# Kernel tuning notes

Hardware: AMD Instinct MI355X
Metric: run time of the kernel (lower is better)

## Reference

```python
import jax, jax.numpy as jnp
import numpy as np
from jax import lax

B, H, W, CIN = 16, 96, 320, 32
N_ACTIVE = 200000
COUT = 256
FC_IN = (H // 8) * (W // 8) * 128  # 12*40*128 = 61440


def _conv(x, w, b):
    # stride-2, pad-1, 3x3 conv in NCHW / OIHW layout
    y = lax.conv_general_dilated(x, w, (2, 2), [(1, 1), (1, 1)],
                                 dimension_numbers=('NCHW', 'OIHW', 'NCHW'))
    return y + b[None, :, None, None]


def _maxpool3(x):
    # 3x3 maxpool, stride 1, pad 1 (NCHW)
    return lax.reduce_window(x, -jnp.inf, lax.max,
                             (1, 1, 3, 3), (1, 1, 1, 1),
                             [(0, 0), (0, 0), (1, 1), (1, 1)])


def setup_inputs() -> dict:
    key = jax.random.key(0)
    ks = jax.random.split(key, 12)
    input_feat = jax.random.normal(ks[0], (B, H, W, CIN), dtype=jnp.float32)
    cb = jax.random.randint(ks[1], (N_ACTIVE, 1), 0, B)
    cy = jax.random.randint(ks[2], (N_ACTIVE, 1), 0, H)
    cx = jax.random.randint(ks[3], (N_ACTIVE, 1), 0, W)
    spconv_coords = jnp.concatenate([cb, cy, cx], axis=1).astype(jnp.int32)
    w1 = jax.random.normal(ks[4], (32, CIN, 3, 3), dtype=jnp.float32) * (1.0 / np.sqrt(CIN * 9))
    b1 = jax.random.normal(ks[5], (32,), dtype=jnp.float32) * 0.01
    w2 = jax.random.normal(ks[6], (64, 32, 3, 3), dtype=jnp.float32) * (1.0 / np.sqrt(32 * 9))
    b2 = jax.random.normal(ks[7], (64,), dtype=jnp.float32) * 0.01
    w3 = jax.random.normal(ks[8], (128, 64, 3, 3), dtype=jnp.float32) * (1.0 / np.sqrt(64 * 9))
    b3 = jax.random.normal(ks[9], (128,), dtype=jnp.float32) * 0.01
    fc_w = jax.random.normal(ks[10], (COUT, FC_IN), dtype=jnp.float32) * (1.0 / np.sqrt(FC_IN))
    fc_b = jax.random.normal(ks[11], (COUT,), dtype=jnp.float32) * 0.01
    return {"input_feat": input_feat, "spconv_coords": spconv_coords,
            "w1": w1, "b1": b1, "w2": w2, "b2": b2, "w3": w3, "b3": b3,
            "fc_w": fc_w, "fc_b": fc_b}


def reference(input_feat, spconv_coords, w1, b1, w2, b2, w3, b3, fc_w, fc_b):
    bi = spconv_coords[:, 0]
    yi = spconv_coords[:, 1]
    xi = spconv_coords[:, 2]
    # gather active-site features, then scatter into a dense NHWC grid
    feats = input_feat[bi, yi, xi]                       # [N, CIN]
    dense = jnp.zeros_like(input_feat).at[bi, yi, xi].set(feats)
    x = dense.transpose(0, 3, 1, 2)                      # [B, CIN, H, W]
    x = jax.nn.relu(_maxpool3(_conv(x, w1, b1)))         # [B, 32, H/2, W/2]
    x = jax.nn.relu(_maxpool3(_conv(x, w2, b2)))         # [B, 64, H/4, W/4]
    x = jax.nn.relu(_maxpool3(_conv(x, w3, b3)))         # [B, 128, H/8, W/8]
    x = x.reshape(x.shape[0], -1)                        # [B, FC_IN]
    return jax.nn.relu(x @ fc_w.T + fc_b)                # [B, COUT]
```

## Files before the change

### kernel.cpp

```cpp
#include <hip/hip_runtime.h>

#define NB 16
#define NH 96
#define NW 320
#define NCIN 32

#define FC_K 61440
#define FC_KC 120
#define FC_NCHUNK 512

typedef __attribute__((ext_vector_type(8))) short short8;
typedef __attribute__((ext_vector_type(4))) float f32x4;

__device__ inline unsigned short f2bf(float f) {
    union { float f; unsigned int u; } v; v.f = f;
    unsigned int r = v.u + 0x7FFF + ((v.u >> 16) & 1);
    return (unsigned short)(r >> 16);
}

__global__ __launch_bounds__(256) void setup_all(const float* __restrict__ w1,
                                                 const float* __restrict__ w2,
                                                 const float* __restrict__ w3,
                                                 unsigned short* __restrict__ f1,
                                                 unsigned short* __restrict__ f2,
                                                 unsigned short* __restrict__ f3,
                                                 const int* __restrict__ coords,
                                                 const float* __restrict__ input,
                                                 unsigned short* __restrict__ inBf,
                                                 int n) {
    if (blockIdx.x < 396) {
        int i = blockIdx.x * 256 + threadIdx.x;
        if (i < 9216) {
            int j = i & 7, lane = (i >> 3) & 63, nt = (i >> 9) & 1, tap = i >> 10;
            int ic = ((lane >> 4) * 8) + j, oc = nt * 16 + (lane & 15);
            f1[i] = f2bf(w1[(oc * 32 + ic) * 9 + tap]);
        } else if (i < 27648) {
            int v = i - 9216;
            int j = v & 7, lane = (v >> 3) & 63, nt = (v >> 9) & 3, tap = v >> 11;
            int ic = ((lane >> 4) * 8) + j, oc = nt * 16 + (lane & 15);
            f2[v] = f2bf(w2[(oc * 32 + ic) * 9 + tap]);
        } else if (i < 101376) {
            int v = i - 27648;
            int j = v & 7, lane = (v >> 3) & 63, nt = (v >> 9) & 7, kk = v >> 12;
            int tap = kk >> 1, ks = kk & 1;
            int ic = ks * 32 + ((lane >> 4) * 8) + j, oc = nt * 16 + (lane & 15);
            f3[v] = f2bf(w3[(oc * 64 + ic) * 9 + tap]);
        }
    } else {
        int i = (blockIdx.x - 396) * 256 + threadIdx.x;
        if (i >= n * 4) return;
        int ci = i >> 2, q = i & 3;
        int b = coords[ci * 3 + 0], y = coords[ci * 3 + 1], x = coords[ci * 3 + 2];
        long base = ((long)((b * NH + y) * NW + x)) * NCIN + q * 8;
        const float4* src = (const float4*)(input + base);
        float4 v0 = src[0], v1 = src[1];
        union { short8 s8; unsigned short us[8]; } o;
        o.us[0] = f2bf(v0.x); o.us[1] = f2bf(v0.y); o.us[2] = f2bf(v0.z); o.us[3] = f2bf(v0.w);
        o.us[4] = f2bf(v1.x); o.us[5] = f2bf(v1.y); o.us[6] = f2bf(v1.z); o.us[7] = f2bf(v1.w);
        *(short8*)(inBf + base) = o.s8;
    }
}

template<int IC, int OC, int NL, int IH, int IW, int OH, int OW>
__global__ __launch_bounds__(256) void conv_mfma(
    const unsigned short* __restrict__ inPtr,
    const unsigned short* __restrict__ wfrag,
    const float* __restrict__ bias,
    float* __restrict__ out)
{
    constexpr int KS = IC / 32;
    constexpr int NT = OC / 16;
    constexpr int NG = NT / NL;
    constexpr int NSTRIPS = NB * OH * OW / 16;

    const int wid  = (blockIdx.x * 256 + threadIdx.x) >> 6;
    const int lane = threadIdx.x & 63;
    const int ntb  = (wid % NG) * NL;
    const int s    = wid / NG;
    if (s >= NSTRIPS) return;
    const int quad = lane >> 4;
    const int lm   = lane & 15;

    const int p0 = s * 16;
    const int posA = p0 + lm;
    const int b  = posA / (OH * OW);
    const int rr = posA % (OH * OW);
    const int oy = rr / OW, ox = rr % OW;
    const int iy0 = oy * 2 - 1, ix0 = ox * 2 - 1;

    int cell[9];
    bool okb[9];
    #pragma unroll
    for (int t9 = 0; t9 < 9; t9++) {
        const int iy = iy0 + t9 / 3;
        const int ix = ix0 + t9 % 3;
        const bool ok = (iy >= 0) && (iy < IH) && (ix >= 0) && (ix < IW);
        cell[t9] = ok ? ((b * IH + iy) * IW + ix) : 0;
        okb[t9] = ok;
    }

    short8 zero8;
    #pragma unroll
    for (int j = 0; j < 8; j++) zero8[j] = 0;

    f32x4 acc[NL][2];
    #pragma unroll
    for (int nl = 0; nl < NL; nl++)
        #pragma unroll
        for (int pp = 0; pp < 2; pp++)
            acc[nl][pp] = (f32x4){0.f, 0.f, 0.f, 0.f};

    #pragma unroll 1
    for (int ks = 0; ks < KS; ks++) {
        short8 av[9];
        #pragma unroll
        for (int t9 = 0; t9 < 9; t9++) {
            short8 v = *(const short8*)(inPtr + (long)cell[t9] * IC + ks * 32 + quad * 8);
            av[t9] = okb[t9] ? v : zero8;
        }
        #pragma unroll
        for (int nl = 0; nl < NL; nl++) {
            #pragma unroll
            for (int t9 = 0; t9 < 9; t9++) {
                short8 bf = *(const short8*)(wfrag + (((t9 * KS + ks) * NT + ntb + nl) * 64 + lane) * 8);
                if (t9 & 1) acc[nl][1] = __builtin_amdgcn_mfma_f32_16x16x32_bf16(av[t9], bf, acc[nl][1], 0, 0, 0);
                else        acc[nl][0] = __builtin_amdgcn_mfma_f32_16x16x32_bf16(av[t9], bf, acc[nl][0], 0, 0, 0);
            }
        }
    }

    const long rowBase = (long)p0 + quad * 4;
    #pragma unroll
    for (int nl = 0; nl < NL; nl++) {
        const int oc = (ntb + nl) * 16 + lm;
        const float bv = bias[oc];
        #pragma unroll
        for (int reg = 0; reg < 4; reg++)
            out[(rowBase + reg) * OC + oc] = acc[nl][0][reg] + acc[nl][1][reg] + bv;
    }
}

template<int C, int HH, int WW, bool BF16OUT>
__global__ __launch_bounds__(256) void maxpool3_relu(const float* __restrict__ in, void* __restrict__ outv) {
    constexpr int C4 = C / 4;
    int i = blockIdx.x * blockDim.x + threadIdx.x;
    if (i >= NB * HH * WW * C4) return;
    int c = i % C4;
    int x = (i / C4) % WW;
    int y = (i / (C4 * WW)) % HH;
    int b = i / (C4 * WW * HH);
    float4 m = make_float4(-3.0e38f, -3.0e38f, -3.0e38f, -3.0e38f);
    #pragma unroll
    for (int dy = -1; dy <= 1; dy++) {
        int yy = y + dy;
        if (yy < 0 || yy >= HH) continue;
        #pragma unroll
        for (int dx = -1; dx <= 1; dx++) {
            int xx = x + dx;
            if (xx < 0 || xx >= WW) continue;
            float4 v = ((const float4*)in)[((b * HH + yy) * WW + xx) * C4 + c];
            m.x = fmaxf(m.x, v.x);
            m.y = fmaxf(m.y, v.y);
            m.z = fmaxf(m.z, v.z);
            m.w = fmaxf(m.w, v.w);
        }
    }
    m.x = fmaxf(m.x, 0.f);
    m.y = fmaxf(m.y, 0.f);
    m.z = fmaxf(m.z, 0.f);
    m.w = fmaxf(m.w, 0.f);
    if (BF16OUT) {
        ushort4 o;
        o.x = f2bf(m.x); o.y = f2bf(m.y); o.z = f2bf(m.z); o.w = f2bf(m.w);
        ((ushort4*)outv)[i] = o;
    } else {
        ((float4*)outv)[i] = m;
    }
}

__global__ __launch_bounds__(256) void transpose_fc(const float* __restrict__ in, float* __restrict__ xT) {
    __shared__ float tile_s[32 * 16 * 17];
    const int pt = blockIdx.x % 30;
    const int ct = blockIdx.x / 30;
    const int pos0 = pt * 16, c0 = ct * 32;
    const int t = threadIdx.x;
    {
        const int b = t / 16, pl = t % 16;
        const float4* src = (const float4*)(in + ((long)(b * 480 + pos0 + pl)) * 128 + c0);
        #pragma unroll
        for (int q = 0; q < 8; q++) {
            float4 v = src[q];
            tile_s[((4 * q + 0) * 16 + pl) * 17 + b] = v.x;
            tile_s[((4 * q + 1) * 16 + pl) * 17 + b] = v.y;
            tile_s[((4 * q + 2) * 16 + pl) * 17 + b] = v.z;
            tile_s[((4 * q + 3) * 16 + pl) * 17 + b] = v.w;
        }
    }
    __syncthreads();
    {
        const int w = t / 64, l = t % 64;
        const int pl2 = l / 4, b4 = l % 4;
        #pragma unroll
        for (int i = 0; i < 8; i++) {
            int cl = w + 4 * i;
            const float* ls = &tile_s[(cl * 16 + pl2) * 17 + 4 * b4];
            float4 v = make_float4(ls[0], ls[1], ls[2], ls[3]);
            *(float4*)(xT + ((long)(c0 + cl) * 480 + pos0 + pl2) * 16 + 4 * b4) = v;
        }
    }
}

__global__ __launch_bounds__(256) void fc_main(const float* __restrict__ xT,
                                               const float* __restrict__ fw,
                                               float* __restrict__ partial)
{
    const int c  = blockIdx.x;
    const int oc = threadIdx.x;
    const int k0 = c * FC_KC;

    const float4* wp = (const float4*)(fw + (long)oc * FC_K + k0);
    float4 w[30];
    #pragma unroll
    for (int i = 0; i < 30; i++) w[i] = wp[i];

    float acc[16];
    #pragma unroll
    for (int b = 0; b < 16; b++) acc[b] = 0.f;

    const float* xb = xT + (long)k0 * 16;
    #pragma unroll
    for (int g = 0; g < 30; g++) {
        #pragma unroll
        for (int j = 0; j < 4; j++) {
            const float wv = (j == 0) ? w[g].x : (j == 1) ? w[g].y : (j == 2) ? w[g].z : w[g].w;
            const float* xp = xb + (g * 4 + j) * 16;
            #pragma unroll
            for (int b = 0; b < 16; b++)
                acc[b] = fmaf(wv, xp[b], acc[b]);
        }
    }

    float4* pp = (float4*)(partial + ((long)c * 256 + oc) * 16);
    pp[0] = make_float4(acc[0],  acc[1],  acc[2],  acc[3]);
    pp[1] = make_float4(acc[4],  acc[5],  acc[6],  acc[7]);
    pp[2] = make_float4(acc[8],  acc[9],  acc[10], acc[11]);
    pp[3] = make_float4(acc[12], acc[13], acc[14], acc[15]);
}

__global__ __launch_bounds__(256) void fc_reduce(const float* __restrict__ partial,
                                                 const float* __restrict__ fcb,
                                                 float* __restrict__ out)
{
    __shared__ float red[16][17];
    const int oc = blockIdx.x;
    const int ol = threadIdx.x & 15;
    const int st = threadIdx.x >> 4;
    float s = 0.f;
    #pragma unroll
    for (int j = 0; j < 32; j++)
        s += partial[(long)(st + 16 * j) * 4096 + oc * 16 + ol];
    red[st][ol] = s;
    __syncthreads();
    if (threadIdx.x < 16) {
        float tot = fcb[oc];
        #pragma unroll
        for (int k = 0; k < 16; k++) tot += red[k][threadIdx.x];
        out[threadIdx.x * 256 + oc] = fmaxf(tot, 0.f);
    }
}

extern "C" void kernel_launch(void* const* d_in, const int* in_sizes, int n_in,
                              void* d_out, int out_size, void* d_ws, size_t ws_size,
                              hipStream_t stream) {
    const float* input  = (const float*)d_in[0];
    const int*   coords = (const int*)d_in[1];
    const float* w1 = (const float*)d_in[2];
    const float* b1 = (const float*)d_in[3];
    const float* w2 = (const float*)d_in[4];
    const float* b2 = (const float*)d_in[5];
    const float* w3 = (const float*)d_in[6];
    const float* b3 = (const float*)d_in[7];
    const float* fcw = (const float*)d_in[8];
    const float* fcb = (const float*)d_in[9];
    float* outp = (float*)d_out;

    const int n_active = in_sizes[1] / 3;

    char* ws = (char*)d_ws;
    unsigned short* wf1 = (unsigned short*)ws;
    unsigned short* wf2 = wf1 + 9216;
    unsigned short* wf3 = wf2 + 18432;
    unsigned short* inBf = (unsigned short*)(ws + 204800);
    char* regA = ws + 204800 + 31457280;
    char* regB = regA + 15728640;
    float* partial = (float*)(regB + 7864320);

    float*          conv1o  = (float*)regA;
    unsigned short* pool1bf = (unsigned short*)regB;
    float*          conv2o  = (float*)regA;
    unsigned short* pool2bf = (unsigned short*)regB;
    float*          conv3o  = (float*)regA;
    float*          pool3f  = (float*)regB;
    float*          xT      = (float*)regA;

    hipMemsetAsync(inBf, 0, 31457280, stream);
    const int scatterBlocks = (n_active * 4 + 255) / 256;
    setup_all<<<396 + scatterBlocks, 256, 0, stream>>>(w1, w2, w3, wf1, wf2, wf3,
                                                       coords, input, inBf, n_active);

    conv_mfma<32, 32, 2, 96, 320, 48, 160>
        <<<1920, 256, 0, stream>>>(inBf, wf1, b1, conv1o);
    maxpool3_relu<32, 48, 160, true><<<3840, 256, 0, stream>>>(conv1o, pool1bf);

    conv_mfma<32, 64, 2, 48, 160, 24, 80>
        <<<960, 256, 0, stream>>>(pool1bf, wf2, b2, conv2o);
    maxpool3_relu<64, 24, 80, true><<<1920, 256, 0, stream>>>(conv2o, pool2bf);

    conv_mfma<64, 128, 2, 24, 80, 12, 40>
        <<<480, 256, 0, stream>>>(pool2bf, wf3, b3, conv3o);
    maxpool3_relu<128, 12, 40, false><<<960, 256, 0, stream>>>(conv3o, pool3f);

    transpose_fc<<<120, 256, 0, stream>>>(pool3f, xT);
    fc_main<<<FC_NCHUNK, 256, 0, stream>>>(xT, fcw, partial);
    fc_reduce<<<256, 256, 0, stream>>>(partial, fcb, outp);
}
```

Before: 243.8 us.

## Restructure FC partial kernel with LDS-staged activations and 4-way k split

After: 242.4 us. About the same (-0.6%).

```diff
diff --git a/kernel.cpp b/kernel.cpp
--- a/kernel.cpp
+++ b/kernel.cpp
@@ -210,41 +210,82 @@
     }
 }
 
-__global__ __launch_bounds__(256) void fc_main(const float* __restrict__ xT,
-                                               const float* __restrict__ fw,
-                                               float* __restrict__ partial)
+__global__ __launch_bounds__(256, 2) void fc_main(const float* __restrict__ xT,
+                                                  const float* __restrict__ fw,
+                                                  float* __restrict__ partial)
 {
-    const int c  = blockIdx.x;
-    const int oc = threadIdx.x;
-    const int k0 = c * FC_KC;
-
-    const float4* wp = (const float4*)(fw + (long)oc * FC_K + k0);
-    float4 w[30];
-    #pragma unroll
-    for (int i = 0; i < 30; i++) w[i] = wp[i];
-
-    float acc[16];
-    #pragma unroll
-    for (int b = 0; b < 16; b++) acc[b] = 0.f;
-
-    const float* xb = xT + (long)k0 * 16;
-    #pragma unroll
-    for (int g = 0; g < 30; g++) {
-        #pragma unroll
-        for (int j = 0; j < 4; j++) {
-            const float wv = (j == 0) ? w[g].x : (j == 1) ? w[g].y : (j == 2) ? w[g].z : w[g].w;
-            const float* xp = xb + (g * 4 + j) * 16;
+    __shared__ float x_lds[120 * 20];
+    const int c    = blockIdx.x;
+    const int t    = threadIdx.x;
+    const int q    = t >> 2;
+    const int ksub = t & 3;
+    const int k0   = c * FC_KC;
+
+    float2 w[4][15];
+    #pragma unroll
+    for (int s = 0; s < 4; s++) {
+        const float* wr = fw + (long)(q + 64 * s) * FC_K + k0 + ksub * 2;
+        #pragma unroll
+        for (int g = 0; g < 15; g++)
+            w[s][g] = *(const float2*)(wr + g * 8);
+    }
+
+    for (int i = t; i < 480; i += 256) {
+        int k = i >> 2, b4 = i & 3;
+        float4 v = *(const float4*)(xT + ((long)(k0 + k)) * 16 + b4 * 4);
+        *(float4*)(&x_lds[k * 20 + b4 * 4]) = v;
+    }
+    __syncthreads();
+
+    float acc[4][16];
+    #pragma unroll
+    for (int s = 0; s < 4; s++)
+        #pragma unroll
+        for (int b = 0; b < 16; b++) acc[s][b] = 0.f;
+
+    #pragma unroll
+    for (int g = 0; g < 15; g++) {
+        #pragma unroll
+        for (int j = 0; j < 2; j++) {
+            const int klbase = 8 * g + j;
+            const float* xr = &x_lds[(klbase + 2 * ksub) * 20];
+            f32x4 xv[4];
             #pragma unroll
-            for (int b = 0; b < 16; b++)
-                acc[b] = fmaf(wv, xp[b], acc[b]);
-        }
-    }
-
-    float4* pp = (float4*)(partial + ((long)c * 256 + oc) * 16);
-    pp[0] = make_float4(acc[0],  acc[1],  acc[2],  acc[3]);
-    pp[1] = make_float4(acc[4],  acc[5],  acc[6],  acc[7]);
-    pp[2] = make_float4(acc[8],  acc[9],  acc[10], acc[11]);
-    pp[3] = make_float4(acc[12], acc[13], acc[14], acc[15]);
+            for (int b4 = 0; b4 < 4; b4++)
+                xv[b4] = *(const f32x4*)(xr + 4 * b4);
+            #pragma unroll
+            for (int s = 0; s < 4; s++) {
+                const float wv = (j == 0) ? w[s][g].x : w[s][g].y;
+                #pragma unroll
+                for (int b4 = 0; b4 < 4; b4++)
+                    #pragma unroll
+                    for (int e = 0; e < 4; e++)
+                        acc[s][b4 * 4 + e] = fmaf(wv, xv[b4][e], acc[s][b4 * 4 + e]);
+            }
+        }
+    }
+
+    #pragma unroll
+    for (int s = 0; s < 4; s++)
+        #pragma unroll
+        for (int b = 0; b < 16; b++) {
+            float v = acc[s][b];
+            v += __shfl_xor(v, 1);
+            v += __shfl_xor(v, 2);
+            acc[s][b] = v;
+        }
+
+    if (ksub == 0) {
+        #pragma unroll
+        for (int s = 0; s < 4; s++) {
+            const int oc = q + 64 * s;
+            float4* pp = (float4*)(partial + ((long)c * 256 + oc) * 16);
+            pp[0] = make_float4(acc[s][0],  acc[s][1],  acc[s][2],  acc[s][3]);
+            pp[1] = make_float4(acc[s][4],  acc[s][5],  acc[s][6],  acc[s][7]);
+            pp[2] = make_float4(acc[s][8],  acc[s][9],  acc[s][10], acc[s][11]);
+            pp[3] = make_float4(acc[s][12], acc[s][13], acc[s][14], acc[s][15]);
+        }
+    }
 }
 
 __global__ __launch_bounds__(256) void fc_reduce(const float* __restrict__ partial,
```

## Restructure FC split-K: stage activations in LDS, split K across lanes

Applied to the files above, without the earlier changes.

Result: no change. 242.2 us (-0.7%).

```diff
diff --git a/kernel.cpp b/kernel.cpp
--- a/kernel.cpp
+++ b/kernel.cpp
@@ -6,8 +6,8 @@
 #define NCIN 32
 
 #define FC_K 61440
-#define FC_KC 120
-#define FC_NCHUNK 512
+#define FC_KC 480
+#define FC_NKC 128
 
 typedef __attribute__((ext_vector_type(8))) short short8;
 typedef __attribute__((ext_vector_type(4))) float f32x4;
@@ -210,41 +210,70 @@
     }
 }
 
-__global__ __launch_bounds__(256) void fc_main(const float* __restrict__ xT,
-                                               const float* __restrict__ fw,
-                                               float* __restrict__ partial)
+__global__ __launch_bounds__(256, 2) void fc_main(const float* __restrict__ xT,
+                                                  const float* __restrict__ fw,
+                                                  float* __restrict__ partial)
 {
-    const int c  = blockIdx.x;
-    const int oc = threadIdx.x;
-    const int k0 = c * FC_KC;
-
-    const float4* wp = (const float4*)(fw + (long)oc * FC_K + k0);
-    float4 w[30];
-    #pragma unroll
-    for (int i = 0; i < 30; i++) w[i] = wp[i];
+    __shared__ float x_lds[480 * 20];
+    const int bx   = blockIdx.x;
+    const int kc   = bx & 127;
+    const int ocb  = bx >> 7;
+    const int t    = threadIdx.x;
+    const int q    = t >> 2;
+    const int ksub = t & 3;
+    const int k0   = kc * FC_KC;
+    const int oc   = ocb * 64 + q;
+
+    const float* wr = fw + (long)oc * FC_K + k0 + ksub * 4;
+    f32x4 w[30];
+    #pragma unroll
+    for (int g = 0; g < 30; g++)
+        w[g] = *(const f32x4*)(wr + g * 16);
+
+    for (int i = t; i < 1920; i += 256) {
+        int k = i >> 2, b4 = i & 3;
+        *(float4*)(&x_lds[k * 20 + b4 * 4]) =
+            *(const float4*)(xT + ((long)(k0 + k)) * 16 + b4 * 4);
+    }
+    __syncthreads();
 
     float acc[16];
     #pragma unroll
     for (int b = 0; b < 16; b++) acc[b] = 0.f;
 
-    const float* xb = xT + (long)k0 * 16;
     #pragma unroll
     for (int g = 0; g < 30; g++) {
         #pragma unroll
-        for (int j = 0; j < 4; j++) {
-            const float wv = (j == 0) ? w[g].x : (j == 1) ? w[g].y : (j == 2) ? w[g].z : w[g].w;
-            const float* xp = xb + (g * 4 + j) * 16;
+        for (int e = 0; e < 4; e++) {
+            const float wv = w[g][e];
+            const float* xr = &x_lds[(g * 16 + ksub * 4 + e) * 20];
+            f32x4 xv[4];
             #pragma unroll
-            for (int b = 0; b < 16; b++)
-                acc[b] = fmaf(wv, xp[b], acc[b]);
-        }
-    }
-
-    float4* pp = (float4*)(partial + ((long)c * 256 + oc) * 16);
-    pp[0] = make_float4(acc[0],  acc[1],  acc[2],  acc[3]);
-    pp[1] = make_float4(acc[4],  acc[5],  acc[6],  acc[7]);
-    pp[2] = make_float4(acc[8],  acc[9],  acc[10], acc[11]);
-    pp[3] = make_float4(acc[12], acc[13], acc[14], acc[15]);
+            for (int b4 = 0; b4 < 4; b4++)
+                xv[b4] = *(const f32x4*)(xr + 4 * b4);
+            #pragma unroll
+            for (int b4 = 0; b4 < 4; b4++)
+                #pragma unroll
+                for (int el = 0; el < 4; el++)
+                    acc[b4 * 4 + el] = fmaf(wv, xv[b4][el], acc[b4 * 4 + el]);
+        }
+    }
+
+    #pragma unroll
+    for (int b = 0; b < 16; b++) {
+        float v = acc[b];
+        v += __shfl_xor(v, 1);
+        v += __shfl_xor(v, 2);
+        acc[b] = v;
+    }
+
+    if (ksub == 0) {
+        float4* pp = (float4*)(partial + ((long)kc * 256 + oc) * 16);
+        pp[0] = make_float4(acc[0],  acc[1],  acc[2],  acc[3]);
+        pp[1] = make_float4(acc[4],  acc[5],  acc[6],  acc[7]);
+        pp[2] = make_float4(acc[8],  acc[9],  acc[10], acc[11]);
+        pp[3] = make_float4(acc[12], acc[13], acc[14], acc[15]);
+    }
 }
 
 __global__ __launch_bounds__(256) void fc_reduce(const float* __restrict__ partial,
@@ -257,7 +286,7 @@
     const int st = threadIdx.x >> 4;
     float s = 0.f;
     #pragma unroll
-    for (int j = 0; j < 32; j++)
+    for (int j = 0; j < 8; j++)
         s += partial[(long)(st + 16 * j) * 4096 + oc * 16 + ol];
     red[st][ol] = s;
     __syncthreads();
@@ -321,6 +350,6 @@
     maxpool3_relu<128, 12, 40, false><<<960, 256, 0, stream>>>(conv3o, pool3f);
 
     transpose_fc<<<120, 256, 0, stream>>>(pool3f, xT);
-    fc_main<<<FC_NCHUNK, 256, 0, stream>>>(xT, fcw, partial);
+    fc_main<<<4 * FC_NKC, 256, 0, stream>>>(xT, fcw, partial);
     fc_reduce<<<256, 256, 0, stream>>>(partial, fcb, outp);
 }
```
